# Performance work log

Measured on AMD Instinct MI355X. Metric: run time of the kernel, lower is better.

The kernel has to match this reference:

```python
import jax, jax.numpy as jnp
import numpy as np

N = 8192        # number of points (dense-cdist branch: N <= 8192)
D = 384         # encoding dim
ALPHA = 5.0     # frequency scale applied to A
RADIUS = 0.2    # ball radius (applied to the (y,z) coords pts[:,1:])


def setup_inputs() -> dict:
    key = jax.random.key(0)
    k1, k2 = jax.random.split(key)
    pts = jax.random.normal(k1, (N, 3), dtype=jnp.float32)
    # A = stack of 3 standard-normal rows, scaled by alpha (strict_standard_normal ~ randn)
    A = jax.random.normal(k2, (3, D), dtype=jnp.float32) * ALPHA
    return {"pts": pts, "A": A}


def reference(pts, A):
    d = A.shape[1]
    sqrt_d = jnp.asarray(d, pts.dtype) ** 0.5
    # --- radius-ball adjacency over the last two coordinates (pts[:,1:]) ---
    xy = pts[:, 1:]                                   # (n, 2)
    sq = jnp.sum(xy * xy, axis=1)                     # (n,)
    d2 = sq[:, None] + sq[None, :] - 2.0 * (xy @ xy.T)  # squared pairwise dist (n, n)
    J = (d2 < RADIUS * RADIUS).astype(pts.dtype)      # (n, n) 0/1 adjacency
    # --- complex kernel features ---
    pA = pts @ A                                      # (n, d)
    c, s = jnp.cos(pA), jnp.sin(pA)                   # real/imag of exp(i*pA)
    # neighbor sum: G = J @ [cos|sin]
    Gre = J @ c                                       # (n, d)
    Gim = J @ s                                       # (n, d)
    # complex divide by exp(i*pA), then row-normalize to norm sqrt(d)
    G = jax.lax.complex(Gre, Gim) / jax.lax.complex(c, s)  # (n, d) complex64
    nrm = jnp.sqrt(jnp.sum(jnp.real(G * jnp.conj(G)), axis=-1, keepdims=True))
    return G / nrm.astype(G.dtype) * sqrt_d
```

## Files before the change

### kernel.cpp

```cpp
#include <hip/hip_runtime.h>
#include <hip/hip_fp16.h>

#define NPTS  8192
#define DDIM  384
#define ROWS  8
#define NBLK  (NPTS / ROWS)
#define UCAP  1536
#define NTHR  512
#define NSLOT 8
#define NC    52
#define NCELL (NC * NC)
#define GY0   -5.2005f
#define GHINV 4.99750124937531f


__device__ __forceinline__ int cell_of(float a, float b)
{
    int c1 = (int)floorf((a - GY0) * GHINV);
    int c2 = (int)floorf((b - GY0) * GHINV);
    c1 = min(NC - 1, max(0, c1));
    c2 = min(NC - 1, max(0, c2));
    return c1 * NC + c2;
}

__device__ __forceinline__ __half2 u2h(unsigned u)
{
    union { unsigned u; __half2 h; } v; v.u = u; return v.h;
}
__device__ __forceinline__ unsigned h2u(__half2 h)
{
    union { unsigned u; __half2 h; } v; v.h = h; return v.u;
}

__global__ __launch_bounds__(1024)
void setup_kernel(const float* __restrict__ pts, int* __restrict__ cellStart,
                  int* __restrict__ perm, float2* __restrict__ xyS)
{
    __shared__ int cnt[NCELL];
    __shared__ int wsum[16];
    const int t    = threadIdx.x;
    const int lane = t & 63, wid = t >> 6;

    for (int c = t; c < NCELL; c += 1024) cnt[c] = 0;
    __syncthreads();
    for (int n = t; n < NPTS; n += 1024)
        atomicAdd(&cnt[cell_of(pts[3 * n + 1], pts[3 * n + 2])], 1);
    __syncthreads();

    const int base = t * 3;
    int s = 0;
    for (int c = base; c < base + 3 && c < NCELL; ++c) s += cnt[c];

    int v = s;
    #pragma unroll
    for (int off = 1; off < 64; off <<= 1) {
        int u = __shfl_up(v, off, 64);
        if (lane >= off) v += u;
    }
    if (lane == 63) wsum[wid] = v;
    __syncthreads();
    if (wid == 0 && lane < 16) {
        int x = wsum[lane];
        #pragma unroll
        for (int off = 1; off < 16; off <<= 1) {
            int u = __shfl_up(x, off, 64);
            if (lane >= off) x += u;
        }
        wsum[lane] = x;
    }
    __syncthreads();
    int acc = v - s + (wid ? wsum[wid - 1] : 0);

    for (int c = base; c < base + 3 && c < NCELL; ++c) {
        int val = cnt[c];
        cellStart[c] = acc;
        cnt[c] = acc;
        acc += val;
    }
    if (t == 0) cellStart[NCELL] = NPTS;
    __syncthreads();

    for (int n = t; n < NPTS; n += 1024) {
        float a = pts[3 * n + 1];
        float b = pts[3 * n + 2];
        int pos = atomicAdd(&cnt[cell_of(a, b)], 1);
        perm[pos] = n;
        xyS[pos]  = make_float2(a, b);
    }
}

__global__ __launch_bounds__(DDIM)
void cs_kernel(const float* __restrict__ pts, const float* __restrict__ A,
               const int* __restrict__ perm, __half2* __restrict__ csS)
{
    const int t  = threadIdx.x;
    const int r0 = blockIdx.x * 8;
    const float a0 = A[t];
    const float a1 = A[DDIM + t];
    const float a2 = A[2 * DDIM + t];
    #pragma unroll
    for (int i = 0; i < 8; ++i) {
        const int r = r0 + i;
        const int n = perm[r];
        const float p0 = pts[3 * n + 0];
        const float p1 = pts[3 * n + 1];
        const float p2 = pts[3 * n + 2];
        const float pa = fmaf(p2, a2, fmaf(p1, a1, __fmul_rn(p0, a0)));
        csS[r * DDIM + t] = __floats2half2_rn(__cosf(pa), __sinf(pa));
    }
}

__global__ __launch_bounds__(NTHR)
void row_kernel(const __half2* __restrict__ csS, const float2* __restrict__ xyS,
                const int* __restrict__ perm, const int* __restrict__ cellStart,
                float* __restrict__ out)
{
    __shared__ int   ulist[UCAP];
    __shared__ int   ucnt;
    __shared__ uint2 partl[NSLOT][64][6];
    __shared__ float red[2][NSLOT];

    const int bid = blockIdx.x;
    const int xcd = bid & 7, q = bid >> 3;
    const int ch  = q >> 4, w = q & 15;
    const int blk = (((ch << 3) + xcd) << 4) + w;
    const int r0  = blk * ROWS;

    const int t  = threadIdx.x;
    const int ks = t >> 6;
    const int cg = t & 63;

    if (t == 0) ucnt = 0;
    __syncthreads();

    float rx[ROWS], ry[ROWS], rs[ROWS];
    #pragma unroll
    for (int rr = 0; rr < ROWS; ++rr) {
        const float2 p = xyS[r0 + rr];
        rx[rr] = p.x; ry[rr] = p.y;
        rs[rr] = __fadd_rn(__fmul_rn(p.x, p.x), __fmul_rn(p.y, p.y));
    }

    int c1lo = NC - 1, c1hi = 0, c2lo = NC - 1, c2hi = 0;
    #pragma unroll
    for (int rr = 0; rr < ROWS; ++rr) {
        int c1 = (int)floorf((rx[rr] - GY0) * GHINV);
        int c2 = (int)floorf((ry[rr] - GY0) * GHINV);
        c1 = min(NC - 1, max(0, c1)); c2 = min(NC - 1, max(0, c2));
        c1lo = min(c1lo, c1); c1hi = max(c1hi, c1);
        c2lo = min(c2lo, c2); c2hi = max(c2hi, c2);
    }
    c1lo = max(0, c1lo - 1); c1hi = min(NC - 1, c1hi + 1);
    c2lo = max(0, c2lo - 1); c2hi = min(NC - 1, c2hi + 1);

    for (int cr = c1lo; cr <= c1hi; ++cr) {
        const int qlo = cellStart[cr * NC + c2lo];
        const int qhi = cellStart[cr * NC + c2hi + 1];
        for (int q0 = qlo + ks * 64; q0 < qhi; q0 += NTHR) {
            const int qq = q0 + cg;
            int bits = 0;
            if (qq < qhi) {
                const float2 pj  = xyS[qq];
                const float  sqj = __fadd_rn(__fmul_rn(pj.x, pj.x),
                                             __fmul_rn(pj.y, pj.y));
                #pragma unroll
                for (int rr = 0; rr < ROWS; ++rr) {
                    const float dot = fmaf(ry[rr], pj.y, __fmul_rn(rx[rr], pj.x));
                    const float d2  = __fsub_rn(__fadd_rn(rs[rr], sqj),
                                                __fmul_rn(2.0f, dot));
                    if (d2 < 0.04f) bits |= (1 << rr);
                }
            }
            const unsigned long long msk = __ballot(bits != 0);
            int wbase = 0;
            const int wcnt = __popcll(msk);
            if (cg == 0 && wcnt) wbase = atomicAdd(&ucnt, wcnt);
            wbase = __shfl(wbase, 0, 64);
            if (bits) {
                const int pos = wbase +
                    __popcll(msk & ((1ull << cg) - 1ull));
                if (pos < UCAP) ulist[pos] = qq | (bits << 13);
            }
        }
    }
    __syncthreads();
    const int U = ucnt < UCAP ? ucnt : UCAP;

    const char* base = (const char*)csS;
    const int   b0   = cg * 24;

    __half2 acc[ROWS][6];
    #pragma unroll
    for (int rr = 0; rr < ROWS; ++rr)
        #pragma unroll
        for (int c = 0; c < 6; ++c) acc[rr][c] = u2h(0);

    int k = 0;
    for (; k + 16 <= U; k += 16) {
        const int pkA = __builtin_amdgcn_readfirstlane(ulist[k + ks]);
        const int pkB = __builtin_amdgcn_readfirstlane(ulist[k + 8 + ks]);
        const int jA = pkA & 0x1FFF, mA = pkA >> 13;
        const int jB = pkB & 0x1FFF, mB = pkB >> 13;
        const char* rA = base + jA * 1536 + b0;
        const char* rB = base + jB * 1536 + b0;
        const uint2 wA0 = *(const uint2*)(rA);
        const uint2 wA1 = *(const uint2*)(rA + 8);
        const uint2 wA2 = *(const uint2*)(rA + 16);
        const uint2 wB0 = *(const uint2*)(rB);
        const uint2 wB1 = *(const uint2*)(rB + 8);
        const uint2 wB2 = *(const uint2*)(rB + 16);
        #pragma unroll
        for (int rr = 0; rr < ROWS; ++rr) {
            if (mA & (1 << rr)) {
                acc[rr][0] = __hadd2(acc[rr][0], u2h(wA0.x));
                acc[rr][1] = __hadd2(acc[rr][1], u2h(wA0.y));
                acc[rr][2] = __hadd2(acc[rr][2], u2h(wA1.x));
                acc[rr][3] = __hadd2(acc[rr][3], u2h(wA1.y));
                acc[rr][4] = __hadd2(acc[rr][4], u2h(wA2.x));
                acc[rr][5] = __hadd2(acc[rr][5], u2h(wA2.y));
            }
        }
        #pragma unroll
        for (int rr = 0; rr < ROWS; ++rr) {
            if (mB & (1 << rr)) {
                acc[rr][0] = __hadd2(acc[rr][0], u2h(wB0.x));
                acc[rr][1] = __hadd2(acc[rr][1], u2h(wB0.y));
                acc[rr][2] = __hadd2(acc[rr][2], u2h(wB1.x));
                acc[rr][3] = __hadd2(acc[rr][3], u2h(wB1.y));
                acc[rr][4] = __hadd2(acc[rr][4], u2h(wB2.x));
                acc[rr][5] = __hadd2(acc[rr][5], u2h(wB2.y));
            }
        }
    }
    for (; k < U; k += NSLOT) {
        if (k + ks < U) {
            const int pkA = __builtin_amdgcn_readfirstlane(ulist[k + ks]);
            const int jA = pkA & 0x1FFF, mA = pkA >> 13;
            const char* rA = base + jA * 1536 + b0;
            const uint2 wA0 = *(const uint2*)(rA);
            const uint2 wA1 = *(const uint2*)(rA + 8);
            const uint2 wA2 = *(const uint2*)(rA + 16);
            #pragma unroll
            for (int rr = 0; rr < ROWS; ++rr) {
                if (mA & (1 << rr)) {
                    acc[rr][0] = __hadd2(acc[rr][0], u2h(wA0.x));
                    acc[rr][1] = __hadd2(acc[rr][1], u2h(wA0.y));
                    acc[rr][2] = __hadd2(acc[rr][2], u2h(wA1.x));
                    acc[rr][3] = __hadd2(acc[rr][3], u2h(wA1.y));
                    acc[rr][4] = __hadd2(acc[rr][4], u2h(wA2.x));
                    acc[rr][5] = __hadd2(acc[rr][5], u2h(wA2.y));
                }
            }
        }
    }

    for (int rr = 0; rr < ROWS; rr += 2) {
        partl[ks][cg][0] = make_uint2(h2u(acc[rr][0]),     h2u(acc[rr][1]));
        partl[ks][cg][1] = make_uint2(h2u(acc[rr][2]),     h2u(acc[rr][3]));
        partl[ks][cg][2] = make_uint2(h2u(acc[rr][4]),     h2u(acc[rr][5]));
        partl[ks][cg][3] = make_uint2(h2u(acc[rr + 1][0]), h2u(acc[rr + 1][1]));
        partl[ks][cg][4] = make_uint2(h2u(acc[rr + 1][2]), h2u(acc[rr + 1][3]));
        partl[ks][cg][5] = make_uint2(h2u(acc[rr + 1][4]), h2u(acc[rr + 1][5]));
        __syncthreads();

        float reA = 0.f, imA = 0.f, reB = 0.f, imB = 0.f;
        if (t < DDIM) {
            const int sc = t / 6, comp = t % 6;
            #pragma unroll
            for (int s = 0; s < NSLOT; ++s) {
                const uint2 wwA = partl[s][sc][comp >> 1];
                const uint2 wwB = partl[s][sc][3 + (comp >> 1)];
                const float2 fA = __half22float2(u2h((comp & 1) ? wwA.y : wwA.x));
                const float2 fB = __half22float2(u2h((comp & 1) ? wwB.y : wwB.x));
                reA += fA.x; imA += fA.y;
                reB += fB.x; imB += fB.y;
            }
        }

        float pA = fmaf(reA, reA, imA * imA);
        float pB = fmaf(reB, reB, imB * imB);
        #pragma unroll
        for (int off = 32; off > 0; off >>= 1) {
            pA += __shfl_down(pA, off, 64);
            pB += __shfl_down(pB, off, 64);
        }
        if ((t & 63) == 0) { red[0][t >> 6] = pA; red[1][t >> 6] = pB; }
        __syncthreads();
        const float totA = ((red[0][0] + red[0][1]) + (red[0][2] + red[0][3]))
                         + ((red[0][4] + red[0][5]) + (red[0][6] + red[0][7]));
        const float totB = ((red[1][0] + red[1][1]) + (red[1][2] + red[1][3]))
                         + ((red[1][4] + red[1][5]) + (red[1][6] + red[1][7]));
        const float sclA = 19.59591794226543f / sqrtf(totA);
        const float sclB = 19.59591794226543f / sqrtf(totB);

        if (t < DDIM) {
            const float2 ciA = __half22float2(csS[(r0 + rr) * DDIM + t]);
            const float2 ciB = __half22float2(csS[(r0 + rr + 1) * DDIM + t]);
            const float  GrA = fmaf(reA, ciA.x, imA * ciA.y);
            const float  GrB = fmaf(reB, ciB.x, imB * ciB.y);
            out[perm[r0 + rr] * DDIM + t]     = GrA * sclA;
            out[perm[r0 + rr + 1] * DDIM + t] = GrB * sclB;
        }
        __syncthreads();
    }
}

extern "C" void kernel_launch(void* const* d_in, const int* in_sizes, int n_in,
                              void* d_out, int out_size, void* d_ws, size_t ws_size,
                              hipStream_t stream)
{
    const float* pts = (const float*)d_in[0];
    const float* A   = (const float*)d_in[1];
    if (n_in >= 2 && in_sizes[0] == 3 * DDIM && in_sizes[1] == NPTS * 3) {
        pts = (const float*)d_in[1];
        A   = (const float*)d_in[0];
    }
    char* ws = (char*)d_ws;
    __half2* csS       = (__half2*)(ws + 0);
    float2*  xyS       = (float2*)(ws + 12582912);
    int*     perm      = (int*)(ws + 12648448);
    int*     cellStart = (int*)(ws + 12681216);
    float*   out       = (float*)d_out;

    setup_kernel<<<1, 1024, 0, stream>>>(pts, cellStart, perm, xyS);
    cs_kernel<<<NPTS / 8, DDIM, 0, stream>>>(pts, A, perm, csS);
    row_kernel<<<NBLK, NTHR, 0, stream>>>(csS, xyS, perm, cellStart, out);
}
```

Before: 66.37 us.

## Split single-block grid setup into parallel bin, prefix and scatter kernels

Replaces the one-block setup kernel, which binned, prefix-summed and scattered all points serially within a single workgroup, with a memset, a multi-block binning kernel using global atomics, a single-block prefix kernel and a multi-block scatter kernel. The aim is to spread binning and scattering across many CUs instead of one. In exchange it adds three extra launches plus a memset, and moves the atomics from shared memory to global memory.

```diff
diff --git a/kernel.cpp b/kernel.cpp
--- a/kernel.cpp
+++ b/kernel.cpp
@@ -32,24 +32,28 @@
     union { unsigned u; __half2 h; } v; v.h = h; return v.u;
 }
 
+
+__global__ void bin_kernel(const float* __restrict__ pts, int* __restrict__ cellCnt)
+{
+    const int n = blockIdx.x * 256 + threadIdx.x;
+    if (n < NPTS)
+        atomicAdd(&cellCnt[cell_of(pts[3 * n + 1], pts[3 * n + 2])], 1);
+}
+
 __global__ __launch_bounds__(1024)
-void setup_kernel(const float* __restrict__ pts, int* __restrict__ cellStart,
-                  int* __restrict__ perm, float2* __restrict__ xyS)
-{
-    __shared__ int cnt[NCELL];
+void prefix_kernel(const int* __restrict__ cellCnt,
+                   int* __restrict__ cellStart, int* __restrict__ cellCur)
+{
     __shared__ int wsum[16];
     const int t    = threadIdx.x;
     const int lane = t & 63, wid = t >> 6;
 
-    for (int c = t; c < NCELL; c += 1024) cnt[c] = 0;
-    __syncthreads();
-    for (int n = t; n < NPTS; n += 1024)
-        atomicAdd(&cnt[cell_of(pts[3 * n + 1], pts[3 * n + 2])], 1);
-    __syncthreads();
-
     const int base = t * 3;
-    int s = 0;
-    for (int c = base; c < base + 3 && c < NCELL; ++c) s += cnt[c];
+    int c0v = 0, c1v = 0, c2v = 0;
+    if (base     < NCELL) c0v = cellCnt[base];
+    if (base + 1 < NCELL) c1v = cellCnt[base + 1];
+    if (base + 2 < NCELL) c2v = cellCnt[base + 2];
+    const int s = c0v + c1v + c2v;
 
     int v = s;
     #pragma unroll
@@ -71,19 +75,21 @@
     __syncthreads();
     int acc = v - s + (wid ? wsum[wid - 1] : 0);
 
-    for (int c = base; c < base + 3 && c < NCELL; ++c) {
-        int val = cnt[c];
-        cellStart[c] = acc;
-        cnt[c] = acc;
-        acc += val;
-    }
+    if (base < NCELL)     { cellStart[base]     = acc; cellCur[base]     = acc; acc += c0v; }
+    if (base + 1 < NCELL) { cellStart[base + 1] = acc; cellCur[base + 1] = acc; acc += c1v; }
+    if (base + 2 < NCELL) { cellStart[base + 2] = acc; cellCur[base + 2] = acc; }
     if (t == 0) cellStart[NCELL] = NPTS;
-    __syncthreads();
-
-    for (int n = t; n < NPTS; n += 1024) {
-        float a = pts[3 * n + 1];
-        float b = pts[3 * n + 2];
-        int pos = atomicAdd(&cnt[cell_of(a, b)], 1);
+}
+
+__global__ void scatter_kernel(const float* __restrict__ pts,
+                               int* __restrict__ cellCur,
+                               int* __restrict__ perm, float2* __restrict__ xyS)
+{
+    const int n = blockIdx.x * 256 + threadIdx.x;
+    if (n < NPTS) {
+        const float a = pts[3 * n + 1];
+        const float b = pts[3 * n + 2];
+        const int pos = atomicAdd(&cellCur[cell_of(a, b)], 1);
         perm[pos] = n;
         xyS[pos]  = make_float2(a, b);
     }
@@ -320,9 +326,14 @@
     float2*  xyS       = (float2*)(ws + 12582912);
     int*     perm      = (int*)(ws + 12648448);
     int*     cellStart = (int*)(ws + 12681216);
+    int*     cellCnt   = (int*)(ws + 12693504);
+    int*     cellCur   = (int*)(ws + 12705792);
     float*   out       = (float*)d_out;
 
-    setup_kernel<<<1, 1024, 0, stream>>>(pts, cellStart, perm, xyS);
+    hipMemsetAsync(cellCnt, 0, NCELL * sizeof(int), stream);
+    bin_kernel<<<NPTS / 256, 256, 0, stream>>>(pts, cellCnt);
+    prefix_kernel<<<1, 1024, 0, stream>>>(cellCnt, cellStart, cellCur);
+    scatter_kernel<<<NPTS / 256, 256, 0, stream>>>(pts, cellCur, perm, xyS);
     cs_kernel<<<NPTS / 8, DDIM, 0, stream>>>(pts, A, perm, csS);
     row_kernel<<<NBLK, NTHR, 0, stream>>>(csS, xyS, perm, cellStart, out);
 }
```

After: 66.91 us. Within noise of the previous version (+0.8%).
